# Kernel optimization log

Measured on AMD Instinct MI355X. Metric: run time of the kernel, lower is better.

Reference implementation:

```python
import jax, jax.numpy as jnp
import numpy as np

# CIN config: input_dim (num_fields) = 32, cross_layer_sizes = [128, 128, 128], split_half = True
NUM_FIELDS = 32
EMBED_DIM = 16
BATCH = 4096
CROSS_SIZES = [128, 128, 128]


def setup_inputs() -> dict:
    key = jax.random.key(0)
    ks = jax.random.split(key, 8)
    x = jax.random.normal(ks[0], (BATCH, NUM_FIELDS, EMBED_DIM), dtype=jnp.float32)
    # Conv1d(kernel_size=1) weights: (out_ch, in_ch) + bias (out_ch,)
    prev = NUM_FIELDS
    inp = {"x": x}
    for i, cs in enumerate(CROSS_SIZES):
        in_ch = NUM_FIELDS * prev
        scale = 1.0 / np.sqrt(in_ch)
        inp[f"W{i}"] = jax.random.uniform(ks[1 + 2 * i], (cs, in_ch), dtype=jnp.float32, minval=-scale, maxval=scale)
        inp[f"b{i}"] = jax.random.uniform(ks[2 + 2 * i], (cs,), dtype=jnp.float32, minval=-scale, maxval=scale)
        prev = cs // 2  # split_half (applied after all but last, but prev for next conv uses halved size)
    return inp


def _cin_forward(x, Ws, bs):
    # x: (B, F, E)
    x0 = x
    h = x
    xs = []
    n_layers = len(Ws)
    for i in range(n_layers):
        B, F, E = x0.shape
        G = h.shape[1]
        # outer product over field dims -> (B, F*G, E)
        z = (x0[:, :, None, :] * h[:, None, :, :]).reshape(B, F * G, E)
        # 1x1 conv == channel matmul; bias broadcast over embed dim; relu
        y = jax.nn.relu(jnp.einsum('oc,bce->boe', Ws[i], z) + bs[i][None, :, None])
        if i != n_layers - 1:
            half = y.shape[1] // 2
            x_keep, h = y[:, :half, :], y[:, half:, :]
        else:
            x_keep, h = y, y
        xs.append(x_keep)
    return jnp.sum(jnp.concatenate(xs, axis=1), axis=2)  # (B, fc_input_dim)


def reference(x, W0, b0, W1, b1, W2, b2):
    return _cin_forward(x, [W0, W1, W2], [b0, b1, b2])
```

## Files before the change

### kernel.cpp

```cpp
#include <hip/hip_runtime.h>

typedef _Float16 half_t;
typedef _Float16 v8h __attribute__((ext_vector_type(8)));
typedef float v4f __attribute__((ext_vector_type(4)));

#define XTP 40
#define HP  72

__global__ __launch_bounds__(256) void prep_w_all(const float* __restrict__ W0,
                                                  const float* __restrict__ W1,
                                                  const float* __restrict__ W2,
                                                  half_t* __restrict__ w0h,
                                                  half_t* __restrict__ w1h,
                                                  half_t* __restrict__ w2h) {
  int i = blockIdx.x * 256 + threadIdx.x;
  const float* src; half_t* dst; int ktot; int ksh; int j;
  if (i < 16384)      { src = W0; dst = w0h; ktot = 1024; ksh = 7; j = i; }
  else if (i < 49152) { src = W1; dst = w1h; ktot = 2048; ksh = 8; j = i - 16384; }
  else                { src = W2; dst = w2h; ktot = 2048; ksh = 8; j = i - 49152; }
  int o = j >> ksh, k8 = j & ((1 << ksh) - 1);
  const float* s = src + (size_t)o * ktot + k8 * 8;
  float4 f0 = *(const float4*)s;
  float4 f1 = *(const float4*)(s + 4);
  union { half_t h[8]; uint4 u; } pk;
  pk.h[0] = (half_t)f0.x; pk.h[1] = (half_t)f0.y; pk.h[2] = (half_t)f0.z; pk.h[3] = (half_t)f0.w;
  pk.h[4] = (half_t)f1.x; pk.h[5] = (half_t)f1.y; pk.h[6] = (half_t)f1.z; pk.h[7] = (half_t)f1.w;
  size_t di = ((size_t)(((o >> 4) << ksh) + k8) * 128) + (size_t)(o & 15) * 8;
  *(uint4*)(dst + di) = pk.u;
}

template <int G, int KTOT, int KEEP, int OUT_BASE, bool H_OUT, bool H_IS_X>
__device__ __forceinline__ void layer(const half_t* __restrict__ wgt,
                                      const float* __restrict__ bias,
                                      const half_t* __restrict__ xt_lds,
                                      half_t* __restrict__ h_lds,
                                      float* __restrict__ out,
                                      size_t b0, int tid) {
  constexpr int SPO  = (G == 64) ? 16 : 8;
  constexpr int NSEL = (G == 64) ? 2 : 1;
  const int lane = tid & 63;
  const int wv = tid >> 6;
  const int e16 = lane & 15;
  const int kq = lane >> 4;

  __syncthreads();

  int lrow[4];
#pragma unroll
  for (int ni = 0; ni < 4; ++ni) lrow[ni] = ni * 16 + e16;

  const half_t* hb = H_IS_X ? xt_lds : h_lds;
  const int hpitch = H_IS_X ? XTP : HP;
  v8h hreg[4][NSEL];
#pragma unroll
  for (int ni = 0; ni < 4; ++ni)
#pragma unroll
    for (int s = 0; s < NSEL; ++s)
      hreg[ni][s] = *(const v8h*)(hb + lrow[ni] * hpitch + s * 32 + kq * 8);

  __syncthreads();

  const half_t* wl = wgt + (size_t)wv * (KTOT * 16) + kq * 128 + e16 * 8;
  v8h a_cur = *(const v8h*)(wl);
  v8h a_nxt = *(const v8h*)(wl + 512);
  wl += 1024;

  v4f acc[4] = {};
  v8h xv[4];

  auto step = [&](v8h a, int t) {
    const int j   = (G == 64) ? (t >> 1) : t;
    const int sel = (G == 64) ? (t & 1) : 0;
#pragma unroll
    for (int ni = 0; ni < 4; ++ni) {
      v8h bfr = hreg[ni][sel] * xv[ni][j];
      acc[ni] = __builtin_amdgcn_mfma_f32_16x16x32_f16(a, bfr, acc[ni], 0, 0, 0);
    }
  };

#pragma unroll 1
  for (int oct = 0; oct < 3; ++oct) {
#pragma unroll
    for (int ni = 0; ni < 4; ++ni)
      xv[ni] = *(const v8h*)(xt_lds + lrow[ni] * XTP + oct * 8);
#pragma unroll
    for (int t = 0; t < SPO; t += 2) {
      v8h a0 = a_cur; a_cur = *(const v8h*)(wl);
      step(a0, t);
      v8h a1 = a_nxt; a_nxt = *(const v8h*)(wl + 512);
      wl += 1024;
      step(a1, t + 1);
    }
  }

  {
#pragma unroll
    for (int ni = 0; ni < 4; ++ni)
      xv[ni] = *(const v8h*)(xt_lds + lrow[ni] * XTP + 3 * 8);
#pragma unroll
    for (int t = 0; t < SPO - 2; t += 2) {
      v8h a0 = a_cur; a_cur = *(const v8h*)(wl);
      step(a0, t);
      v8h a1 = a_nxt; a_nxt = *(const v8h*)(wl + 512);
      wl += 1024;
      step(a1, t + 1);
    }
    step(a_cur, SPO - 2);
    step(a_nxt, SPO - 1);
  }

  const int o_base = wv * 16 + kq * 4;
  float4 b4 = *(const float4*)(bias + o_base);
#pragma unroll
  for (int ni = 0; ni < 4; ++ni) {
    float v[4];
#pragma unroll
    for (int r = 0; r < 4; ++r)
      v[r] = fmaxf(acc[ni][r] + (&b4.x)[r], 0.0f);
    if (H_OUT && wv >= 4) {
      union { half_t h[4]; uint2 u; } pk;
#pragma unroll
      for (int r = 0; r < 4; ++r) pk.h[r] = (half_t)v[r];
      *(uint2*)(h_lds + lrow[ni] * HP + (o_base - 64)) = pk.u;
    }
    if (wv * 16 < KEEP) {
#pragma unroll
      for (int r = 0; r < 4; ++r) {
        float sv = v[r];
        sv += __shfl_xor(sv, 1);
        sv += __shfl_xor(sv, 2);
        sv += __shfl_xor(sv, 4);
        sv += __shfl_xor(sv, 8);
        if (e16 == 0) out[(b0 + ni) * 256 + OUT_BASE + o_base + r] = sv;
      }
    }
  }
}

__global__ __launch_bounds__(512, 4) void cin_fused(const float* __restrict__ x,
                                                    const half_t* __restrict__ w0h,
                                                    const half_t* __restrict__ w1h,
                                                    const half_t* __restrict__ w2h,
                                                    const float* __restrict__ b0p,
                                                    const float* __restrict__ b1p,
                                                    const float* __restrict__ b2p,
                                                    float* __restrict__ out) {
  __shared__ __align__(16) half_t xt_lds[64 * XTP];
  __shared__ __align__(16) half_t h_lds[64 * HP];

  const int tid = threadIdx.x;
  const size_t b0 = (size_t)blockIdx.x * 4;

  {
    int idx = tid * 4;
    float4 v = *(const float4*)(x + b0 * 512 + idx);
    int e = idx & 15, f = (idx >> 4) & 31, b = idx >> 9;
    half_t* d = xt_lds + (b * 16 + e) * XTP + f;
    d[0 * XTP] = (half_t)v.x;
    d[1 * XTP] = (half_t)v.y;
    d[2 * XTP] = (half_t)v.z;
    d[3 * XTP] = (half_t)v.w;
  }

  layer<32, 1024, 64, 0, true, true>(w0h, b0p, xt_lds, h_lds, out, b0, tid);
  layer<64, 2048, 64, 64, true, false>(w1h, b1p, xt_lds, h_lds, out, b0, tid);
  layer<64, 2048, 128, 128, false, false>(w2h, b2p, xt_lds, h_lds, out, b0, tid);
}

extern "C" void kernel_launch(void* const* d_in, const int* in_sizes, int n_in,
                              void* d_out, int out_size, void* d_ws, size_t ws_size,
                              hipStream_t stream) {
  const float* x  = (const float*)d_in[0];
  const float* W0 = (const float*)d_in[1];
  const float* b0 = (const float*)d_in[2];
  const float* W1 = (const float*)d_in[3];
  const float* b1 = (const float*)d_in[4];
  const float* W2 = (const float*)d_in[5];
  const float* b2 = (const float*)d_in[6];
  float* out = (float*)d_out;
  char* ws = (char*)d_ws;

  half_t* w0h = (half_t*)(ws);
  half_t* w1h = (half_t*)(ws + (256u << 10));
  half_t* w2h = (half_t*)(ws + (768u << 10));

  prep_w_all<<<320, 256, 0, stream>>>(W0, W1, W2, w0h, w1h, w2h);
  cin_fused<<<1024, 512, 0, stream>>>(x, w0h, w1h, w2h, b0, b1, b2, out);
}
```

Before: 162.9 us.

## Switch CIN kernel to 32x32x16 MFMA with 8 batches per block

Replaces the 16x16x32 MFMA tiling with 32x32x16 MFMA. Each wave now covers 32 output channels across 4 batch samples, and each block processes 8 batches instead of 4, so every weight fragment loaded from global memory is reused across twice as many samples. The weight prep layout is rearranged to match the new A-operand fragment order, and the x*h broadcast multiply now uses packed half2 ops on duplicated scalars. The cost is larger LDS use per block, a larger per-wave accumulator footprint, and only half as many blocks (512), which could lower occupancy or leave CUs less evenly loaded.

```diff
diff --git a/kernel.cpp b/kernel.cpp
--- a/kernel.cpp
+++ b/kernel.cpp
@@ -2,7 +2,8 @@
 
 typedef _Float16 half_t;
 typedef _Float16 v8h __attribute__((ext_vector_type(8)));
-typedef float v4f __attribute__((ext_vector_type(4)));
+typedef _Float16 h2  __attribute__((ext_vector_type(2)));
+typedef float f32x16 __attribute__((ext_vector_type(16)));
 
 #define XTP 40
 #define HP  72
@@ -25,8 +26,22 @@
   union { half_t h[8]; uint4 u; } pk;
   pk.h[0] = (half_t)f0.x; pk.h[1] = (half_t)f0.y; pk.h[2] = (half_t)f0.z; pk.h[3] = (half_t)f0.w;
   pk.h[4] = (half_t)f1.x; pk.h[5] = (half_t)f1.y; pk.h[6] = (half_t)f1.z; pk.h[7] = (half_t)f1.w;
-  size_t di = ((size_t)(((o >> 4) << ksh) + k8) * 128) + (size_t)(o & 15) * 8;
+  int st = o >> 5, r = o & 31;
+  int t = k8 >> 2, w = k8 & 3;
+  int kk = w >> 1, hi = w & 1;
+  size_t di = ((size_t)(st * (ktot >> 5) + t) * 1024) + kk * 512 + (hi * 32 + r) * 8;
   *(uint4*)(dst + di) = pk.u;
+}
+
+__device__ __forceinline__ unsigned dup_lo(unsigned w) { return (w << 16) | (w & 0xffffu); }
+__device__ __forceinline__ unsigned dup_hi(unsigned w) { return (w >> 16) | (w & 0xffff0000u); }
+
+__device__ __forceinline__ v8h mul_bcast(v8h h, unsigned xx) {
+  union U { v8h v; h2 p[4]; unsigned u[4]; } a, r, x;
+  a.v = h; x.u[0] = xx;
+#pragma unroll
+  for (int i = 0; i < 4; ++i) r.p[i] = a.p[i] * x.p[0];
+  return r.v;
 }
 
 template <int G, int KTOT, int KEEP, int OUT_BASE, bool H_OUT, bool H_IS_X>
@@ -36,102 +51,138 @@
                                       half_t* __restrict__ h_lds,
                                       float* __restrict__ out,
                                       size_t b0, int tid) {
-  constexpr int SPO  = (G == 64) ? 16 : 8;
-  constexpr int NSEL = (G == 64) ? 2 : 1;
+  constexpr int STEPS = KTOT / 32;
+  constexpr int SPO   = (G == 64) ? 16 : 8;
+  constexpr int NCH   = (G == 64) ? 4 : 2;
   const int lane = tid & 63;
-  const int wv = tid >> 6;
+  const int wv  = tid >> 6;
+  const int ms  = wv & 3;
+  const int ng  = wv >> 2;
   const int e16 = lane & 15;
-  const int kq = lane >> 4;
+  const int bl  = (lane >> 4) & 1;
+  const int khi = lane >> 5;
 
   __syncthreads();
 
-  int lrow[4];
-#pragma unroll
-  for (int ni = 0; ni < 4; ++ni) lrow[ni] = ni * 16 + e16;
+  int lrow[2];
+#pragma unroll
+  for (int nt = 0; nt < 2; ++nt) lrow[nt] = (ng * 4 + nt * 2 + bl) * 16 + e16;
 
   const half_t* hb = H_IS_X ? xt_lds : h_lds;
   const int hpitch = H_IS_X ? XTP : HP;
-  v8h hreg[4][NSEL];
-#pragma unroll
-  for (int ni = 0; ni < 4; ++ni)
-#pragma unroll
-    for (int s = 0; s < NSEL; ++s)
-      hreg[ni][s] = *(const v8h*)(hb + lrow[ni] * hpitch + s * 32 + kq * 8);
+  v8h hreg[2][NCH];
+#pragma unroll
+  for (int nt = 0; nt < 2; ++nt)
+#pragma unroll
+    for (int c = 0; c < NCH; ++c) {
+      const int off = (G == 64) ? ((c >> 1) * 32 + (c & 1) * 16 + khi * 8)
+                                : (c * 16 + khi * 8);
+      hreg[nt][c] = *(const v8h*)(hb + lrow[nt] * hpitch + off);
+    }
 
   __syncthreads();
 
-  const half_t* wl = wgt + (size_t)wv * (KTOT * 16) + kq * 128 + e16 * 8;
-  v8h a_cur = *(const v8h*)(wl);
-  v8h a_nxt = *(const v8h*)(wl + 512);
-  wl += 1024;
-
-  v4f acc[4] = {};
-  v8h xv[4];
-
-  auto step = [&](v8h a, int t) {
-    const int j   = (G == 64) ? (t >> 1) : t;
-    const int sel = (G == 64) ? (t & 1) : 0;
-#pragma unroll
-    for (int ni = 0; ni < 4; ++ni) {
-      v8h bfr = hreg[ni][sel] * xv[ni][j];
-      acc[ni] = __builtin_amdgcn_mfma_f32_16x16x32_f16(a, bfr, acc[ni], 0, 0, 0);
+  const half_t* wl = wgt + (size_t)ms * (STEPS * 1024) + lane * 8;
+  v8h a0c = *(const v8h*)(wl);
+  v8h a1c = *(const v8h*)(wl + 512);
+  v8h a0n = *(const v8h*)(wl + 1024);
+  v8h a1n = *(const v8h*)(wl + 1536);
+  wl += 2048;
+
+  f32x16 acc[2] = {};
+  unsigned xwu[2][4];
+
+  auto dostep = [&](v8h a0, v8h a1, int tloc) {
+    const int j = (G == 64) ? (tloc >> 1) : tloc;
+    unsigned xx[2];
+#pragma unroll
+    for (int nt = 0; nt < 2; ++nt) {
+      const unsigned w = xwu[nt][j >> 1];
+      xx[nt] = (j & 1) ? dup_hi(w) : dup_lo(w);
+    }
+#pragma unroll
+    for (int kk = 0; kk < 2; ++kk) {
+      const v8h a = kk ? a1 : a0;
+      const int c = (G == 64) ? ((tloc & 1) * 2 + kk) : kk;
+#pragma unroll
+      for (int nt = 0; nt < 2; ++nt) {
+        v8h bfr = mul_bcast(hreg[nt][c], xx[nt]);
+        acc[nt] = __builtin_amdgcn_mfma_f32_32x32x16_f16(a, bfr, acc[nt], 0, 0, 0);
+      }
     }
   };
 
 #pragma unroll 1
   for (int oct = 0; oct < 3; ++oct) {
 #pragma unroll
-    for (int ni = 0; ni < 4; ++ni)
-      xv[ni] = *(const v8h*)(xt_lds + lrow[ni] * XTP + oct * 8);
-#pragma unroll
-    for (int t = 0; t < SPO; t += 2) {
-      v8h a0 = a_cur; a_cur = *(const v8h*)(wl);
-      step(a0, t);
-      v8h a1 = a_nxt; a_nxt = *(const v8h*)(wl + 512);
-      wl += 1024;
-      step(a1, t + 1);
+    for (int nt = 0; nt < 2; ++nt) {
+      uint4 q = *(const uint4*)(xt_lds + lrow[nt] * XTP + oct * 8);
+      xwu[nt][0] = q.x; xwu[nt][1] = q.y; xwu[nt][2] = q.z; xwu[nt][3] = q.w;
+    }
+#pragma unroll
+    for (int tl = 0; tl < SPO; tl += 2) {
+      v8h A0 = a0c, A1 = a1c;
+      a0c = *(const v8h*)(wl);
+      a1c = *(const v8h*)(wl + 512);
+      dostep(A0, A1, tl);
+      v8h B0 = a0n, B1 = a1n;
+      a0n = *(const v8h*)(wl + 1024);
+      a1n = *(const v8h*)(wl + 1536);
+      wl += 2048;
+      dostep(B0, B1, tl + 1);
     }
   }
 
   {
 #pragma unroll
-    for (int ni = 0; ni < 4; ++ni)
-      xv[ni] = *(const v8h*)(xt_lds + lrow[ni] * XTP + 3 * 8);
-#pragma unroll
-    for (int t = 0; t < SPO - 2; t += 2) {
-      v8h a0 = a_cur; a_cur = *(const v8h*)(wl);
-      step(a0, t);
-      v8h a1 = a_nxt; a_nxt = *(const v8h*)(wl + 512);
-      wl += 1024;
-      step(a1, t + 1);
-    }
-    step(a_cur, SPO - 2);
-    step(a_nxt, SPO - 1);
-  }
-
-  const int o_base = wv * 16 + kq * 4;
-  float4 b4 = *(const float4*)(bias + o_base);
-#pragma unroll
-  for (int ni = 0; ni < 4; ++ni) {
-    float v[4];
-#pragma unroll
-    for (int r = 0; r < 4; ++r)
-      v[r] = fmaxf(acc[ni][r] + (&b4.x)[r], 0.0f);
-    if (H_OUT && wv >= 4) {
-      union { half_t h[4]; uint2 u; } pk;
-#pragma unroll
-      for (int r = 0; r < 4; ++r) pk.h[r] = (half_t)v[r];
-      *(uint2*)(h_lds + lrow[ni] * HP + (o_base - 64)) = pk.u;
-    }
-    if (wv * 16 < KEEP) {
-#pragma unroll
-      for (int r = 0; r < 4; ++r) {
-        float sv = v[r];
-        sv += __shfl_xor(sv, 1);
-        sv += __shfl_xor(sv, 2);
-        sv += __shfl_xor(sv, 4);
-        sv += __shfl_xor(sv, 8);
-        if (e16 == 0) out[(b0 + ni) * 256 + OUT_BASE + o_base + r] = sv;
+    for (int nt = 0; nt < 2; ++nt) {
+      uint4 q = *(const uint4*)(xt_lds + lrow[nt] * XTP + 3 * 8);
+      xwu[nt][0] = q.x; xwu[nt][1] = q.y; xwu[nt][2] = q.z; xwu[nt][3] = q.w;
+    }
+#pragma unroll
+    for (int tl = 0; tl < SPO - 2; tl += 2) {
+      v8h A0 = a0c, A1 = a1c;
+      a0c = *(const v8h*)(wl);
+      a1c = *(const v8h*)(wl + 512);
+      dostep(A0, A1, tl);
+      v8h B0 = a0n, B1 = a1n;
+      a0n = *(const v8h*)(wl + 1024);
+      a1n = *(const v8h*)(wl + 1536);
+      wl += 2048;
+      dostep(B0, B1, tl + 1);
+    }
+    dostep(a0c, a1c, SPO - 2);
+    dostep(a0n, a1n, SPO - 1);
+  }
+
+  const int obase0 = ms * 32;
+#pragma unroll
+  for (int nt = 0; nt < 2; ++nt) {
+    const int bb = ng * 4 + nt * 2 + bl;
+#pragma unroll
+    for (int q = 0; q < 4; ++q) {
+      const int ob = obase0 + q * 8 + khi * 4;
+      float4 b4 = *(const float4*)(bias + ob);
+      float v[4];
+#pragma unroll
+      for (int r = 0; r < 4; ++r)
+        v[r] = fmaxf(acc[nt][q * 4 + r] + (&b4.x)[r], 0.0f);
+      if (H_OUT && obase0 >= 64) {
+        union { half_t h[4]; uint2 u; } pk;
+#pragma unroll
+        for (int r = 0; r < 4; ++r) pk.h[r] = (half_t)v[r];
+        *(uint2*)(h_lds + (bb * 16 + e16) * HP + (ob - 64)) = pk.u;
+      }
+      if (obase0 < KEEP) {
+#pragma unroll
+        for (int r = 0; r < 4; ++r) {
+          float sv = v[r];
+          sv += __shfl_xor(sv, 1);
+          sv += __shfl_xor(sv, 2);
+          sv += __shfl_xor(sv, 4);
+          sv += __shfl_xor(sv, 8);
+          if (e16 == 0) out[(b0 + bb) * 256 + OUT_BASE + ob + r] = sv;
+        }
       }
     }
   }
@@ -145,14 +196,15 @@
                                                     const float* __restrict__ b1p,
                                                     const float* __restrict__ b2p,
                                                     float* __restrict__ out) {
-  __shared__ __align__(16) half_t xt_lds[64 * XTP];
-  __shared__ __align__(16) half_t h_lds[64 * HP];
+  __shared__ __align__(16) half_t xt_lds[128 * XTP];
+  __shared__ __align__(16) half_t h_lds[128 * HP];
 
   const int tid = threadIdx.x;
-  const size_t b0 = (size_t)blockIdx.x * 4;
-
-  {
-    int idx = tid * 4;
+  const size_t b0 = (size_t)blockIdx.x * 8;
+
+#pragma unroll
+  for (int i = 0; i < 2; ++i) {
+    int idx = (i * 512 + tid) * 4;
     float4 v = *(const float4*)(x + b0 * 512 + idx);
     int e = idx & 15, f = (idx >> 4) & 31, b = idx >> 9;
     half_t* d = xt_lds + (b * 16 + e) * XTP + f;
@@ -185,5 +237,5 @@
   half_t* w2h = (half_t*)(ws + (768u << 10));
 
   prep_w_all<<<320, 256, 0, stream>>>(W0, W1, W2, w0h, w1h, w2h);
-  cin_fused<<<1024, 512, 0, stream>>>(x, w0h, w1h, w2h, b0, b1, b2, out);
-}
+  cin_fused<<<512, 512, 0, stream>>>(x, w0h, w1h, w2h, b0, b1, b2, out);
+}
```

After: 163.3 us. Within noise of the previous version (+0.3%).
